# Performance work log

Hardware: AMD Instinct MI355X
Metric: run time of the kernel (lower is better)

## Reference

```python
import jax, jax.numpy as jnp
import numpy as np

D_K = 512  # module-level global used for the scale factor


def setup_inputs() -> dict:
    key = jax.random.key(0)
    kq, kk, kv, km = jax.random.split(key, 4)
    B, H, L = 4, 8, 1024
    Q = jax.random.normal(kq, (B, H, L, D_K), dtype=jnp.float32)
    K = jax.random.normal(kk, (B, H, L, D_K), dtype=jnp.float32)
    V = jax.random.normal(kv, (B, H, L, D_K), dtype=jnp.float32)
    attn_mask = jax.random.randint(km, (B, H, L, L), 0, 2).astype(jnp.bool_)
    return {"Q": Q, "K": K, "V": V, "attn_mask": attn_mask}


def reference(Q, K, V, attn_mask):
    scale = 1.0 / np.sqrt(D_K).astype(np.float32)
    # [B,H,Lq,Lk]
    scores = jnp.einsum('bhqd,bhkd->bhqk', Q, K) * scale
    scores = jnp.where(attn_mask, jnp.float32(-1e9), scores)
    attn = jax.nn.softmax(scores, axis=-1)
    context = jnp.einsum('bhqk,bhkd->bhqd', attn, V)
    return (context, attn)
```

## Files before the change

kernel.cpp:

```cpp
#include <hip/hip_runtime.h>
#include <hip/hip_bf16.h>

constexpr int BH  = 32;
constexpr int LQ  = 1024;
constexpr int DK  = 512;
constexpr float SCALE = 0.04419417382415922f;

using short8 = __attribute__((ext_vector_type(8))) short;
using f32x4  = __attribute__((ext_vector_type(4))) float;

__device__ __forceinline__ unsigned short cvt_bf16(float x) {
  unsigned int u = __builtin_bit_cast(unsigned int, x);
  u += 0x7FFFu + ((u >> 16) & 1u);
  return (unsigned short)(u >> 16);
}
__device__ __forceinline__ float bf2f(unsigned short s) {
  return __builtin_bit_cast(float, (unsigned int)s << 16);
}
__device__ __forceinline__ unsigned int pack2(float a, float b) {
  return (unsigned int)cvt_bf16(a) | ((unsigned int)cvt_bf16(b) << 16);
}

__device__ __forceinline__ void lds_load16(const void* g, void* l) {
  __builtin_amdgcn_global_load_lds(
      (const __attribute__((address_space(1))) unsigned int*)g,
      (__attribute__((address_space(3))) unsigned int*)l, 16, 0, 0);
}

__global__ __launch_bounds__(256) void cvt2_f32_bf16(
    const float* __restrict__ s0, const float* __restrict__ s1,
    unsigned short* __restrict__ d0, unsigned short* __restrict__ d1, int n8) {
  const float* src = blockIdx.y ? s1 : s0;
  unsigned short* dst = blockIdx.y ? d1 : d0;
  int i = blockIdx.x * 256 + threadIdx.x;
  const int stride = gridDim.x * 256;
  for (; i < n8; i += stride) {
    float4 a = ((const float4*)src)[(size_t)i * 2];
    float4 b = ((const float4*)src)[(size_t)i * 2 + 1];
    unsigned short us[8] __attribute__((aligned(16)));
    us[0]=cvt_bf16(a.x); us[1]=cvt_bf16(a.y); us[2]=cvt_bf16(a.z); us[3]=cvt_bf16(a.w);
    us[4]=cvt_bf16(b.x); us[5]=cvt_bf16(b.y); us[6]=cvt_bf16(b.z); us[7]=cvt_bf16(b.w);
    ((short8*)dst)[i] = *(short8*)us;
  }
}

__global__ __launch_bounds__(512) void qk_v4_kernel(
    const unsigned short* __restrict__ A, const unsigned short* __restrict__ B,
    const int* __restrict__ mask, unsigned short* __restrict__ P,
    float* __restrict__ partials) {
  __shared__ __attribute__((aligned(16))) unsigned short smem[24576];

  int flat = blockIdx.x + 8 * (blockIdx.y + 4 * blockIdx.z);
  flat = (flat % 8) * 128 + flat / 8;
  const int bx = flat % 8;
  const int by = (flat / 8) % 4;
  const int bh = flat / 32;

  const int t = threadIdx.x;
  const int lane = t & 63, wave = t >> 6;
  const int wr = wave >> 1;
  const int wc = wave & 1;
  const int fr = lane & 15, fq = lane >> 4;
  const int m0 = by * 256, n0 = bx * 128;

  const char* Ab = (const char*)A + ((size_t)bh * LQ + m0) * 1024;
  const char* Bb = (const char*)B + ((size_t)bh * LQ + n0) * 1024;

  unsigned int orv = 0;
  {
    const unsigned int* mw = (const unsigned int*)mask;
    #pragma unroll
    for (int i = 0; i < 64; ++i) orv |= mw[i];
  }
  const bool byteMode = (orv > 1u);

  f32x4 acc[4][4];
  #pragma unroll
  for (int i = 0; i < 4; ++i)
    #pragma unroll
    for (int j = 0; j < 4; ++j) acc[i][j] = (f32x4){0.f, 0.f, 0.f, 0.f};

  char* const AsB = (char*)smem;
  char* const BsB = (char*)smem + 32768;

  for (int kt = 0; kt < 8; ++kt) {
    const int kb = kt * 128;
    __syncthreads();
    #pragma unroll
    for (int i = 0; i < 4; ++i) {
      const int p  = i * 8192 + t * 16;
      const int r  = p >> 7;
      const int ch = (p >> 4) & 7;
      lds_load16(Ab + (size_t)r * 1024 + kb + ((ch ^ (r & 7)) << 4),
                 AsB + i * 8192 + wave * 1024);
    }
    #pragma unroll
    for (int i = 0; i < 2; ++i) {
      const int p  = i * 8192 + t * 16;
      const int r  = p >> 7;
      const int ch = (p >> 4) & 7;
      lds_load16(Bb + (size_t)r * 1024 + kb + ((ch ^ (r & 7)) << 4),
                 BsB + i * 8192 + wave * 1024);
    }
    __syncthreads();

    #pragma unroll
    for (int kk = 0; kk < 2; ++kk) {
      short8 a[4], b[4];
      #pragma unroll
      for (int mi = 0; mi < 4; ++mi) {
        const int r  = wr * 64 + mi * 16 + fr;
        const int ch = (kk * 4 + fq) ^ (r & 7);
        a[mi] = *(const short8*)(AsB + r * 128 + ch * 16);
      }
      #pragma unroll
      for (int ni = 0; ni < 4; ++ni) {
        const int r  = wc * 64 + ni * 16 + fr;
        const int ch = (kk * 4 + fq) ^ (r & 7);
        b[ni] = *(const short8*)(BsB + r * 128 + ch * 16);
      }
      #pragma unroll
      for (int mi = 0; mi < 4; ++mi)
        #pragma unroll
        for (int ni = 0; ni < 4; ++ni)
          acc[mi][ni] = __builtin_amdgcn_mfma_f32_16x16x32_bf16(a[mi], b[ni], acc[mi][ni], 0, 0, 0);
    }
  }

  unsigned short* Cs = smem;
  const size_t pbase = (size_t)bh * LQ * LQ;
  #pragma unroll
  for (int h = 0; h < 2; ++h) {
    __syncthreads();
    if ((wr >> 1) == h) {
      #pragma unroll
      for (int mi = 0; mi < 4; ++mi)
        #pragma unroll
        for (int ni = 0; ni < 4; ++ni) {
          const int col = wc * 64 + ni * 16 + fr;
          #pragma unroll
          for (int r = 0; r < 4; ++r) {
            const int rloc = (wr & 1) * 64 + mi * 16 + fq * 4 + r;
            Cs[rloc * 136 + col] = cvt_bf16(__expf(acc[mi][ni][r] * SCALE));
          }
        }
    }
    __syncthreads();
    const int rl = t >> 4;
    const int cl = (t & 15) * 8;
    #pragma unroll
    for (int rb = 0; rb < 4; ++rb) {
      const int rloc = rb * 32 + rl;
      const int rg   = m0 + h * 128 + rloc;
      const size_t gidx = pbase + (size_t)rg * LQ + (n0 + cl);
      short8 sv = *(const short8*)&Cs[rloc * 136 + cl];
      bool mk[8];
      if (byteMode) {
        const unsigned char* mb = (const unsigned char*)mask + gidx;
        uint2 w = *(const uint2*)mb;
        #pragma unroll
        for (int j = 0; j < 4; ++j) mk[j]     = ((w.x >> (8 * j)) & 255u) != 0u;
        #pragma unroll
        for (int j = 0; j < 4; ++j) mk[4 + j] = ((w.y >> (8 * j)) & 255u) != 0u;
      } else {
        int4 w0 = *(const int4*)(mask + gidx);
        int4 w1 = *(const int4*)(mask + gidx + 4);
        mk[0] = w0.x != 0; mk[1] = w0.y != 0; mk[2] = w0.z != 0; mk[3] = w0.w != 0;
        mk[4] = w1.x != 0; mk[5] = w1.y != 0; mk[6] = w1.z != 0; mk[7] = w1.w != 0;
      }
      unsigned short out[8] __attribute__((aligned(16)));
      float s = 0.f;
      #pragma unroll
      for (int j = 0; j < 8; ++j) {
        unsigned short v = mk[j] ? (unsigned short)0 : (unsigned short)sv[j];
        out[j] = v;
        s += bf2f(v);
      }
      *(short8*)(P + gidx) = *(short8*)out;
      s += __shfl_xor(s, 1); s += __shfl_xor(s, 2);
      s += __shfl_xor(s, 4); s += __shfl_xor(s, 8);
      if ((t & 15) == 0)
        partials[((size_t)bh * LQ + rg) * 8 + bx] = s;
    }
  }
}

__global__ __launch_bounds__(256) void pv2f_kernel(
    const unsigned short* __restrict__ P, const float* __restrict__ V,
    const float* __restrict__ partials, float* __restrict__ O,
    float* __restrict__ attn) {
  __shared__ __attribute__((aligned(16))) unsigned short As[8192];
  __shared__ __attribute__((aligned(16))) unsigned short BsV[128 * 72];
  __shared__ float invsL[128];

  int flat = blockIdx.x + 4 * (blockIdx.y + 8 * blockIdx.z);
  flat = (flat % 8) * 128 + flat / 8;
  const int bx = flat % 4;
  const int by = (flat / 4) % 8;
  const int bh = flat / 32;

  const int t = threadIdx.x;
  const int lane = t & 63, wave = t >> 6;
  const int wr = wave >> 1, wc = wave & 1;
  const int fr = lane & 15, fq = lane >> 4;
  const int m0 = by * 128, n0 = bx * 128;

  if (t < 128) {
    const float* pp = partials + ((size_t)bh * LQ + m0 + t) * 8;
    float s = ((pp[0] + pp[1]) + (pp[2] + pp[3])) + ((pp[4] + pp[5]) + (pp[6] + pp[7]));
    invsL[t] = 1.0f / s;
  }

  const char* Ab  = (const char*)P + ((size_t)bh * LQ + m0) * 2048;
  const float* Vb = V + (size_t)bh * LQ * DK + n0;
  float* attnB = attn + ((size_t)bh * LQ + m0) * LQ;

  f32x4 acc[4][4];
  #pragma unroll
  for (int i = 0; i < 4; ++i)
    #pragma unroll
    for (int j = 0; j < 4; ++j) acc[i][j] = (f32x4){0.f, 0.f, 0.f, 0.f};

  const int g  = t >> 5;
  const int nl = t & 31;

  for (int k0 = 0; k0 < LQ; k0 += 64) {
    __syncthreads();
    #pragma unroll
    for (int i = 0; i < 4; ++i) {
      const int p  = i * 4096 + t * 16;
      const int r  = p >> 7;
      const int ch = (p >> 4) & 7;
      const int sw = ((ch ^ (r & 7)) << 4);
      lds_load16(Ab + (size_t)r * 2048 + k0 * 2 + sw, (char*)As + wave * 1024 + i * 4096);
    }
    float vf[8][4];
    #pragma unroll
    for (int i = 0; i < 8; ++i) {
      const size_t rb = (size_t)(k0 + 8 * g + i) * DK;
      #pragma unroll
      for (int jn = 0; jn < 4; ++jn)
        vf[i][jn] = Vb[rb + nl + 32 * jn];
    }
    #pragma unroll
    for (int jn = 0; jn < 4; ++jn) {
      const int n = nl + 32 * jn;
      uint2 w0, w1;
      w0.x = pack2(vf[0][jn], vf[1][jn]); w0.y = pack2(vf[2][jn], vf[3][jn]);
      w1.x = pack2(vf[4][jn], vf[5][jn]); w1.y = pack2(vf[6][jn], vf[7][jn]);
      *(uint2*)((char*)BsV + n * 144 + 16 * g)     = w0;
      *(uint2*)((char*)BsV + n * 144 + 16 * g + 8) = w1;
    }
    __syncthreads();

    if ((k0 >> 8) == bx) {
      #pragma unroll
      for (int rep = 0; rep < 4; ++rep) {
        const int r  = rep * 32 + (t >> 3);
        const int ch = t & 7;
        short8 sv = *(const short8*)((const char*)As + r * 128 + ((ch ^ (r & 7)) << 4));
        const float inv = invsL[r];
        float4 o0, o1;
        o0.x = bf2f((unsigned short)sv[0]) * inv;
        o0.y = bf2f((unsigned short)sv[1]) * inv;
        o0.z = bf2f((unsigned short)sv[2]) * inv;
        o0.w = bf2f((unsigned short)sv[3]) * inv;
        o1.x = bf2f((unsigned short)sv[4]) * inv;
        o1.y = bf2f((unsigned short)sv[5]) * inv;
        o1.z = bf2f((unsigned short)sv[6]) * inv;
        o1.w = bf2f((unsigned short)sv[7]) * inv;
        float* dst = attnB + (size_t)r * LQ + k0 + ch * 8;
        *(float4*)dst       = o0;
        *(float4*)(dst + 4) = o1;
      }
    }

    #pragma unroll
    for (int kk = 0; kk < 2; ++kk) {
      short8 a[4], b[4];
      #pragma unroll
      for (int mi = 0; mi < 4; ++mi) {
        const int r  = wr * 64 + mi * 16 + fr;
        const int ch = (kk * 4 + fq) ^ (r & 7);
        a[mi] = *(const short8*)((const char*)As + r * 128 + ch * 16);
      }
      #pragma unroll
      for (int ni = 0; ni < 4; ++ni) {
        const int r = wc * 64 + ni * 16 + fr;
        b[ni] = *(const short8*)((const char*)BsV + r * 144 + (kk * 4 + fq) * 16);
      }
      #pragma unroll
      for (int mi = 0; mi < 4; ++mi)
        #pragma unroll
        for (int ni = 0; ni < 4; ++ni)
          acc[mi][ni] = __builtin_amdgcn_mfma_f32_16x16x32_bf16(a[mi], b[ni], acc[mi][ni], 0, 0, 0);
    }
  }

  const size_t obase = (size_t)bh * LQ * DK;
  #pragma unroll
  for (int mi = 0; mi < 4; ++mi)
    #pragma unroll
    for (int ni = 0; ni < 4; ++ni) {
      const int col = n0 + wc * 64 + ni * 16 + fr;
      #pragma unroll
      for (int r = 0; r < 4; ++r) {
        const int rloc = wr * 64 + mi * 16 + fq * 4 + r;
        O[obase + (size_t)(m0 + rloc) * DK + col] = acc[mi][ni][r] * invsL[rloc];
      }
    }
}

__global__ __launch_bounds__(256) void qk_mask_kernel(
    const float* __restrict__ Q, const float* __restrict__ Kmat,
    const int* __restrict__ mask, float* __restrict__ S) {
  __shared__ __attribute__((aligned(16))) unsigned short Asf[128][40];
  __shared__ __attribute__((aligned(16))) unsigned short Bsf[128][40];
  const int t = threadIdx.x;
  const int lane = t & 63, wave = t >> 6;
  const int wr = wave >> 1, wc = wave & 1;
  const int fr = lane & 15, fq = lane >> 4;
  const int bh = blockIdx.z;
  const int m0 = blockIdx.y * 128, n0 = blockIdx.x * 128;
  const float* Qb = Q + (size_t)bh * LQ * DK;
  const float* Kb = Kmat + (size_t)bh * LQ * DK;
  unsigned int orv = 0;
  { const unsigned int* mw = (const unsigned int*)mask;
    #pragma unroll
    for (int i = 0; i < 64; ++i) orv |= mw[i]; }
  const bool byteMode = (orv > 1u);
  f32x4 acc[4][4];
  #pragma unroll
  for (int i = 0; i < 4; ++i)
    #pragma unroll
    for (int j = 0; j < 4; ++j) acc[i][j] = (f32x4){0.f,0.f,0.f,0.f};
  const int sr = t >> 1, sc = (t & 1) * 16;
  for (int kd = 0; kd < DK; kd += 32) {
    __syncthreads();
    { const float4* qa = (const float4*)(Qb + (size_t)(m0+sr)*DK + kd + sc);
      float fv[16];
      #pragma unroll
      for (int i = 0; i < 4; ++i) { float4 x = qa[i];
        fv[4*i]=x.x; fv[4*i+1]=x.y; fv[4*i+2]=x.z; fv[4*i+3]=x.w; }
      unsigned short us[16] __attribute__((aligned(16)));
      #pragma unroll
      for (int i = 0; i < 16; ++i) us[i] = cvt_bf16(fv[i]);
      *(short8*)&Asf[sr][sc]   = *(short8*)&us[0];
      *(short8*)&Asf[sr][sc+8] = *(short8*)&us[8]; }
    { const float4* ka = (const float4*)(Kb + (size_t)(n0+sr)*DK + kd + sc);
      float fv[16];
      #pragma unroll
      for (int i = 0; i < 4; ++i) { float4 x = ka[i];
        fv[4*i]=x.x; fv[4*i+1]=x.y; fv[4*i+2]=x.z; fv[4*i+3]=x.w; }
      unsigned short us[16] __attribute__((aligned(16)));
      #pragma unroll
      for (int i = 0; i < 16; ++i) us[i] = cvt_bf16(fv[i]);
      *(short8*)&Bsf[sr][sc]   = *(short8*)&us[0];
      *(short8*)&Bsf[sr][sc+8] = *(short8*)&us[8]; }
    __syncthreads();
    short8 a[4], b[4];
    #pragma unroll
    for (int mi = 0; mi < 4; ++mi) a[mi] = *(const short8*)&Asf[wr*64+mi*16+fr][fq*8];
    #pragma unroll
    for (int ni = 0; ni < 4; ++ni) b[ni] = *(const short8*)&Bsf[wc*64+ni*16+fr][fq*8];
    #pragma unroll
    for (int mi = 0; mi < 4; ++mi)
      #pragma unroll
      for (int ni = 0; ni < 4; ++ni)
        acc[mi][ni] = __builtin_amdgcn_mfma_f32_16x16x32_bf16(a[mi], b[ni], acc[mi][ni], 0, 0, 0);
  }
  const size_t sbase = (size_t)bh * LQ * LQ;
  const unsigned char* mb = (const unsigned char*)mask;
  #pragma unroll
  for (int mi = 0; mi < 4; ++mi)
    #pragma unroll
    for (int ni = 0; ni < 4; ++ni) {
      const int col = n0 + wc*64 + ni*16 + fr;
      #pragma unroll
      for (int r = 0; r < 4; ++r) {
        const int row = m0 + wr*64 + mi*16 + fq*4 + r;
        const size_t idx = sbase + (size_t)row * LQ + col;
        float s = acc[mi][ni][r] * SCALE;
        const bool msk = byteMode ? (mb[idx] != 0) : (mask[idx] != 0);
        S[idx] = msk ? -1e9f : s;
      }
    }
}

__global__ __launch_bounds__(256) void softmax_kernel(float* __restrict__ A) {
  const int row = blockIdx.x;
  float4* rp = (float4*)(A + (size_t)row * LQ);
  const int t = threadIdx.x;
  float4 v = rp[t];
  float m = fmaxf(fmaxf(v.x, v.y), fmaxf(v.z, v.w));
  #pragma unroll
  for (int off = 32; off >= 1; off >>= 1) m = fmaxf(m, __shfl_xor(m, off, 64));
  __shared__ float redm[4];
  const int wv = t >> 6, ln = t & 63;
  if (ln == 0) redm[wv] = m;
  __syncthreads();
  m = fmaxf(fmaxf(redm[0], redm[1]), fmaxf(redm[2], redm[3]));
  float4 e;
  e.x = expf(v.x - m); e.y = expf(v.y - m); e.z = expf(v.z - m); e.w = expf(v.w - m);
  float s = (e.x + e.y) + (e.z + e.w);
  #pragma unroll
  for (int off = 32; off >= 1; off >>= 1) s += __shfl_xor(s, off, 64);
  __shared__ float reds2[4];
  if (ln == 0) reds2[wv] = s;
  __syncthreads();
  s = (reds2[0] + reds2[1]) + (reds2[2] + reds2[3]);
  const float inv = 1.0f / s;
  e.x *= inv; e.y *= inv; e.z *= inv; e.w *= inv;
  rp[t] = e;
}

__global__ __launch_bounds__(256) void pv_kernel(
    const float* __restrict__ P, const float* __restrict__ V, float* __restrict__ O) {
  __shared__ __attribute__((aligned(16))) unsigned short Ps[128][40];
  __shared__ __attribute__((aligned(16))) unsigned short Vtl[128][40];
  const int t = threadIdx.x;
  const int lane = t & 63, wave = t >> 6;
  const int wr = wave >> 1, wc = wave & 1;
  const int fr = lane & 15, fq = lane >> 4;
  const int bh = blockIdx.z;
  const int m0 = blockIdx.y * 128, n0 = blockIdx.x * 128;
  const float* Pb = P + (size_t)bh * LQ * LQ;
  const float* Vb = V + (size_t)bh * LQ * DK;
  f32x4 acc[4][4];
  #pragma unroll
  for (int i = 0; i < 4; ++i)
    #pragma unroll
    for (int j = 0; j < 4; ++j) acc[i][j] = (f32x4){0.f,0.f,0.f,0.f};
  const int sr = t >> 1, sc = (t & 1) * 16;
  const int kk = (t & 15) * 2, nn = (t >> 4) * 8;
  for (int k0 = 0; k0 < LQ; k0 += 32) {
    __syncthreads();
    { const float4* pa = (const float4*)(Pb + (size_t)(m0+sr)*LQ + k0 + sc);
      float fv[16];
      #pragma unroll
      for (int i = 0; i < 4; ++i) { float4 x = pa[i];
        fv[4*i]=x.x; fv[4*i+1]=x.y; fv[4*i+2]=x.z; fv[4*i+3]=x.w; }
      unsigned short us[16] __attribute__((aligned(16)));
      #pragma unroll
      for (int i = 0; i < 16; ++i) us[i] = cvt_bf16(fv[i]);
      *(short8*)&Ps[sr][sc]   = *(short8*)&us[0];
      *(short8*)&Ps[sr][sc+8] = *(short8*)&us[8]; }
    { const float* v0p = Vb + (size_t)(k0+kk)*DK + n0 + nn;
      const float* v1p = v0p + DK;
      float4 a0 = *(const float4*)v0p, a1 = *(const float4*)(v0p+4);
      float4 b0 = *(const float4*)v1p, b1 = *(const float4*)(v1p+4);
      float r0[8] = {a0.x,a0.y,a0.z,a0.w,a1.x,a1.y,a1.z,a1.w};
      float r1[8] = {b0.x,b0.y,b0.z,b0.w,b1.x,b1.y,b1.z,b1.w};
      #pragma unroll
      for (int i = 0; i < 8; ++i) {
        unsigned int pk = (unsigned int)cvt_bf16(r0[i]) | ((unsigned int)cvt_bf16(r1[i]) << 16);
        *(unsigned int*)&Vtl[nn+i][kk] = pk; } }
    __syncthreads();
    short8 a[4], b[4];
    #pragma unroll
    for (int mi = 0; mi < 4; ++mi) a[mi] = *(const short8*)&Ps[wr*64+mi*16+fr][fq*8];
    #pragma unroll
    for (int ni = 0; ni < 4; ++ni) b[ni] = *(const short8*)&Vtl[wc*64+ni*16+fr][fq*8];
    #pragma unroll
    for (int mi = 0; mi < 4; ++mi)
      #pragma unroll
      for (int ni = 0; ni < 4; ++ni)
        acc[mi][ni] = __builtin_amdgcn_mfma_f32_16x16x32_bf16(a[mi], b[ni], acc[mi][ni], 0, 0, 0);
  }
  const size_t obase = (size_t)bh * LQ * DK;
  #pragma unroll
  for (int mi = 0; mi < 4; ++mi)
    #pragma unroll
    for (int ni = 0; ni < 4; ++ni) {
      const int col = n0 + wc*64 + ni*16 + fr;
      #pragma unroll
      for (int r = 0; r < 4; ++r) {
        const int row = m0 + wr*64 + mi*16 + fq*4 + r;
        O[obase + (size_t)row * DK + col] = acc[mi][ni][r];
      }
    }
}

extern "C" void kernel_launch(void* const* d_in, const int* in_sizes, int n_in,
                              void* d_out, int out_size, void* d_ws, size_t ws_size,
                              hipStream_t stream) {
  const float* Q    = (const float*)d_in[0];
  const float* K    = (const float*)d_in[1];
  const float* V    = (const float*)d_in[2];
  const int*   mask = (const int*)d_in[3];

  float* ctx  = (float*)d_out;
  float* attn = ctx + (size_t)BH * LQ * DK;

  const size_t NE = (size_t)BH * LQ * DK;
  const size_t P_BYTES  = (size_t)BH * LQ * LQ * 2;
  const size_t WS_NEED  = P_BYTES + (size_t)BH * LQ * 8 * 4;

  if (ws_size >= WS_NEED) {
    unsigned short* Pp       = (unsigned short*)d_ws;
    float*          partials = (float*)((char*)d_ws + P_BYTES);
    unsigned short* Qb = (unsigned short*)ctx;
    unsigned short* Kb = Qb + NE;

    cvt2_f32_bf16<<<dim3(1024, 2), 256, 0, stream>>>(Q, K, Qb, Kb, (int)(NE / 8));
    qk_v4_kernel<<<dim3(8, 4, BH), 512, 0, stream>>>(Qb, Kb, mask, Pp, partials);
    pv2f_kernel<<<dim3(4, 8, BH), 256, 0, stream>>>(Pp, V, partials, ctx, attn);
  } else {
    qk_mask_kernel<<<dim3(8, 8, BH), 256, 0, stream>>>(Q, K, mask, attn);
    softmax_kernel<<<dim3(BH * LQ), 256, 0, stream>>>(attn);
    pv_kernel<<<dim3(4, 8, BH), 256, 0, stream>>>(attn, V, ctx);
  }
}
```

Before: 224.0 us.

## Split attn normalization into separate interleaved blocks alongside PV GEMM blocks

The fused PV kernel used to write the normalized fp32 attention matrix from inside the GEMM tiles, and only on the k-step that matched each block's column index. That made some blocks do extra store work at different times. Now the 1D grid alternates between two roles: GEMM blocks compute only the context, and new blocks read bf16 P from global memory, scale it by the inverse row sums, and write attn. This is meant to balance the store-heavy work across the machine and overlap it with the MFMA work, at the cost of reading P from global memory a second time.

After: 247.0 us. 1.1x slower.

```diff
diff --git a/kernel.cpp b/kernel.cpp
--- a/kernel.cpp
+++ b/kernel.cpp
@@ -185,7 +185,7 @@
   }
 }
 
-__global__ __launch_bounds__(256) void pv2f_kernel(
+__global__ __launch_bounds__(256) void pv_fin_kernel(
     const unsigned short* __restrict__ P, const float* __restrict__ V,
     const float* __restrict__ partials, float* __restrict__ O,
     float* __restrict__ attn) {
@@ -193,73 +193,32 @@
   __shared__ __attribute__((aligned(16))) unsigned short BsV[128 * 72];
   __shared__ float invsL[128];
 
-  int flat = blockIdx.x + 4 * (blockIdx.y + 8 * blockIdx.z);
-  flat = (flat % 8) * 128 + flat / 8;
-  const int bx = flat % 4;
-  const int by = (flat / 4) % 8;
-  const int bh = flat / 32;
-
   const int t = threadIdx.x;
-  const int lane = t & 63, wave = t >> 6;
-  const int wr = wave >> 1, wc = wave & 1;
-  const int fr = lane & 15, fq = lane >> 4;
-  const int m0 = by * 128, n0 = bx * 128;
-
-  if (t < 128) {
-    const float* pp = partials + ((size_t)bh * LQ + m0 + t) * 8;
-    float s = ((pp[0] + pp[1]) + (pp[2] + pp[3])) + ((pp[4] + pp[5]) + (pp[6] + pp[7]));
-    invsL[t] = 1.0f / s;
-  }
-
-  const char* Ab  = (const char*)P + ((size_t)bh * LQ + m0) * 2048;
-  const float* Vb = V + (size_t)bh * LQ * DK + n0;
-  float* attnB = attn + ((size_t)bh * LQ + m0) * LQ;
-
-  f32x4 acc[4][4];
-  #pragma unroll
-  for (int i = 0; i < 4; ++i)
-    #pragma unroll
-    for (int j = 0; j < 4; ++j) acc[i][j] = (f32x4){0.f, 0.f, 0.f, 0.f};
-
-  const int g  = t >> 5;
-  const int nl = t & 31;
-
-  for (int k0 = 0; k0 < LQ; k0 += 64) {
-    __syncthreads();
-    #pragma unroll
-    for (int i = 0; i < 4; ++i) {
-      const int p  = i * 4096 + t * 16;
-      const int r  = p >> 7;
-      const int ch = (p >> 4) & 7;
-      const int sw = ((ch ^ (r & 7)) << 4);
-      lds_load16(Ab + (size_t)r * 2048 + k0 * 2 + sw, (char*)As + wave * 1024 + i * 4096);
-    }
-    float vf[8][4];
-    #pragma unroll
-    for (int i = 0; i < 8; ++i) {
-      const size_t rb = (size_t)(k0 + 8 * g + i) * DK;
-      #pragma unroll
-      for (int jn = 0; jn < 4; ++jn)
-        vf[i][jn] = Vb[rb + nl + 32 * jn];
-    }
-    #pragma unroll
-    for (int jn = 0; jn < 4; ++jn) {
-      const int n = nl + 32 * jn;
-      uint2 w0, w1;
-      w0.x = pack2(vf[0][jn], vf[1][jn]); w0.y = pack2(vf[2][jn], vf[3][jn]);
-      w1.x = pack2(vf[4][jn], vf[5][jn]); w1.y = pack2(vf[6][jn], vf[7][jn]);
-      *(uint2*)((char*)BsV + n * 144 + 16 * g)     = w0;
-      *(uint2*)((char*)BsV + n * 144 + 16 * g + 8) = w1;
-    }
-    __syncthreads();
-
-    if ((k0 >> 8) == bx) {
-      #pragma unroll
-      for (int rep = 0; rep < 4; ++rep) {
-        const int r  = rep * 32 + (t >> 3);
-        const int ch = t & 7;
-        short8 sv = *(const short8*)((const char*)As + r * 128 + ((ch ^ (r & 7)) << 4));
-        const float inv = invsL[r];
+  const int role = blockIdx.x & 1;
+  const int id   = blockIdx.x >> 1;
+
+  if (role) {
+    const int ch  = id & 1;
+    const int rb64 = (id >> 1) & 15;
+    const int bh  = id >> 5;
+    const int m0  = rb64 * 64;
+    if (t < 64) {
+      const float* pp = partials + ((size_t)bh * LQ + m0 + t) * 8;
+      float s = ((pp[0] + pp[1]) + (pp[2] + pp[3])) + ((pp[4] + pp[5]) + (pp[6] + pp[7]));
+      invsL[t] = 1.0f / s;
+    }
+    __syncthreads();
+    const size_t pbase = (size_t)bh * LQ * LQ;
+    const int c0 = ch * 512;
+    #pragma unroll
+    for (int rb = 0; rb < 4; ++rb) {
+      const int rloc = rb * 16 + (t >> 4);
+      const int row  = m0 + rloc;
+      const float inv = invsL[rloc];
+      const size_t base = pbase + (size_t)row * LQ + c0 + (t & 15) * 8;
+      #pragma unroll
+      for (int j = 0; j < 4; ++j) {
+        short8 sv = *(const short8*)(P + base + j * 128);
         float4 o0, o1;
         o0.x = bf2f((unsigned short)sv[0]) * inv;
         o0.y = bf2f((unsigned short)sv[1]) * inv;
@@ -269,11 +228,70 @@
         o1.y = bf2f((unsigned short)sv[5]) * inv;
         o1.z = bf2f((unsigned short)sv[6]) * inv;
         o1.w = bf2f((unsigned short)sv[7]) * inv;
-        float* dst = attnB + (size_t)r * LQ + k0 + ch * 8;
-        *(float4*)dst       = o0;
-        *(float4*)(dst + 4) = o1;
-      }
-    }
+        *(float4*)(attn + base + j * 128)     = o0;
+        *(float4*)(attn + base + j * 128 + 4) = o1;
+      }
+    }
+    return;
+  }
+
+  int flat = id;
+  flat = (flat % 8) * 128 + flat / 8;
+  const int bx = flat % 4;
+  const int by = (flat / 4) % 8;
+  const int bh = flat / 32;
+
+  const int lane = t & 63, wave = t >> 6;
+  const int wr = wave >> 1, wc = wave & 1;
+  const int fr = lane & 15, fq = lane >> 4;
+  const int m0 = by * 128, n0 = bx * 128;
+
+  if (t < 128) {
+    const float* pp = partials + ((size_t)bh * LQ + m0 + t) * 8;
+    float s = ((pp[0] + pp[1]) + (pp[2] + pp[3])) + ((pp[4] + pp[5]) + (pp[6] + pp[7]));
+    invsL[t] = 1.0f / s;
+  }
+
+  const char* Ab  = (const char*)P + ((size_t)bh * LQ + m0) * 2048;
+  const float* Vb = V + (size_t)bh * LQ * DK + n0;
+
+  f32x4 acc[4][4];
+  #pragma unroll
+  for (int i = 0; i < 4; ++i)
+    #pragma unroll
+    for (int j = 0; j < 4; ++j) acc[i][j] = (f32x4){0.f, 0.f, 0.f, 0.f};
+
+  const int g  = t >> 5;
+  const int nl = t & 31;
+
+  for (int k0 = 0; k0 < LQ; k0 += 64) {
+    __syncthreads();
+    #pragma unroll
+    for (int i = 0; i < 4; ++i) {
+      const int p  = i * 4096 + t * 16;
+      const int r  = p >> 7;
+      const int ch = (p >> 4) & 7;
+      const int sw = ((ch ^ (r & 7)) << 4);
+      lds_load16(Ab + (size_t)r * 2048 + k0 * 2 + sw, (char*)As + wave * 1024 + i * 4096);
+    }
+    float vf[8][4];
+    #pragma unroll
+    for (int i = 0; i < 8; ++i) {
+      const size_t rb = (size_t)(k0 + 8 * g + i) * DK;
+      #pragma unroll
+      for (int jn = 0; jn < 4; ++jn)
+        vf[i][jn] = Vb[rb + nl + 32 * jn];
+    }
+    #pragma unroll
+    for (int jn = 0; jn < 4; ++jn) {
+      const int n = nl + 32 * jn;
+      uint2 w0, w1;
+      w0.x = pack2(vf[0][jn], vf[1][jn]); w0.y = pack2(vf[2][jn], vf[3][jn]);
+      w1.x = pack2(vf[4][jn], vf[5][jn]); w1.y = pack2(vf[6][jn], vf[7][jn]);
+      *(uint2*)((char*)BsV + n * 144 + 16 * g)     = w0;
+      *(uint2*)((char*)BsV + n * 144 + 16 * g + 8) = w1;
+    }
+    __syncthreads();
 
     #pragma unroll
     for (int kk = 0; kk < 2; ++kk) {
@@ -504,7 +522,7 @@
 
     cvt2_f32_bf16<<<dim3(1024, 2), 256, 0, stream>>>(Q, K, Qb, Kb, (int)(NE / 8));
     qk_v4_kernel<<<dim3(8, 4, BH), 512, 0, stream>>>(Qb, Kb, mask, Pp, partials);
-    pv2f_kernel<<<dim3(4, 8, BH), 256, 0, stream>>>(Pp, V, partials, ctx, attn);
+    pv_fin_kernel<<<dim3(2048), 256, 0, stream>>>(Pp, V, partials, ctx, attn);
   } else {
     qk_mask_kernel<<<dim3(8, 8, BH), 256, 0, stream>>>(Q, K, mask, attn);
     softmax_kernel<<<dim3(BH * LQ), 256, 0, stream>>>(attn);
```
